# Kernel tuning notes

Measured on AMD Instinct MI355X. Metric: run time of the kernel, lower is better.

The kernel has to match this reference:

```python
import jax, jax.numpy as jnp
import numpy as np

NUM_ANCHORS = 3
NUM_CLASSES = 3
NUM_BB_ATTR = 9  # x, y, z, h, w, l, im, re, conf
EXP_CLAMP = 1000.0

_ANCHORS = np.array([[11.4, 8.6, 38.7, 0.0, 1.0],
                     [25.4, 11.2, 52.0, 0.0, 1.0],
                     [41.9, 16.2, 75.2, 0.0, 1.0]], dtype=np.float32)


def setup_inputs() -> dict:
    key = jax.random.key(0)
    B, G = 32, 152
    C = NUM_ANCHORS * (NUM_BB_ATTR + NUM_CLASSES)  # 36
    x = jax.random.normal(key, (B, C, G, G), dtype=jnp.float32)
    anchors = jnp.asarray(_ANCHORS)
    return {"x": x, "anchors": anchors, "img_size": 608}


def reference(x, anchors, img_size):
    B, _, G, _ = x.shape
    nA, nC, nbb = NUM_ANCHORS, NUM_CLASSES, NUM_BB_ATTR
    stride = jnp.asarray(img_size, x.dtype) / G

    # [B, nA, 9+nC, G, G] -> [B, nA, G, G, 9+nC]
    pred = x.reshape(B, nA, nbb + nC, G, G).transpose(0, 1, 3, 4, 2)

    pred_x = jax.nn.sigmoid(pred[..., 0])
    pred_y = jax.nn.sigmoid(pred[..., 1])
    pred_z = jax.nn.sigmoid(pred[..., 2])
    pred_h = pred[..., 3]
    pred_w = pred[..., 4]
    pred_l = pred[..., 5]
    pred_im = pred[..., 6]
    pred_re = pred[..., 7]
    pred_conf = jax.nn.sigmoid(pred[..., 8])
    pred_cls = jax.nn.sigmoid(pred[..., 9:])

    # grid offsets: grid_x varies along last (x) axis, grid_y along row axis
    g = jnp.arange(G, dtype=x.dtype)
    grid_x = g[None, None, None, :]   # [1,1,1,G] broadcasts over rows
    grid_y = g[None, None, :, None]   # [1,1,G,1] broadcasts over cols

    scaled = jnp.concatenate([anchors[:, :3] / stride, anchors[:, 3:]], axis=1)
    anchor_h = scaled[:, 0].reshape(1, nA, 1, 1)
    anchor_w = scaled[:, 1].reshape(1, nA, 1, 1)
    anchor_l = scaled[:, 2].reshape(1, nA, 1, 1)

    bx = pred_x + grid_x
    by = pred_y + grid_y
    bz = pred_z
    bh = jnp.minimum(jnp.exp(pred_h), EXP_CLAMP) * anchor_h
    bw = jnp.minimum(jnp.exp(pred_w), EXP_CLAMP) * anchor_w
    bl = jnp.minimum(jnp.exp(pred_l), EXP_CLAMP) * anchor_l

    N = nA * G * G
    flat = lambda t: t.reshape(B, N, 1)
    output = jnp.concatenate([
        flat(bx) * stride, flat(by) * stride,   # xy in image units
        flat(bz),
        flat(bh) * stride, flat(bw) * stride, flat(bl) * stride,
        flat(pred_im), flat(pred_re),
        flat(pred_conf),
        pred_cls.reshape(B, N, nC),
    ], axis=-1)  # [B, nA*G*G, 9+nC]
    return output
```

## Files before the change

kernel.cpp:

```cpp
#include <hip/hip_runtime.h>
#include <math.h>

#define GDIM 152
#define NA 3
#define GG (GDIM * GDIM)
#define EXP_CLAMP 1000.0f
#define NTHREADS 64
#define TILE 256
#define GSTRIDE (TILE + 1)

typedef float floatx4 __attribute__((ext_vector_type(4)));

__device__ __forceinline__ float sigmoidf(float v) {
    return 1.0f / (1.0f + __expf(-v));
}

__device__ __forceinline__ int swz(int e) { return e ^ ((e >> 3) & 7); }

__global__ __launch_bounds__(NTHREADS) void yolo_decode_w64(
    const float* __restrict__ x,
    const float* __restrict__ anchors,
    const int* __restrict__ img_size_p,
    float* __restrict__ out)
{
    __shared__ floatx4 sh[3 * GSTRIDE];

    const int t = threadIdx.x;
    const int tilebase = blockIdx.x * TILE;

    const float stride = (float)(*img_size_p) / (float)GDIM;
    const float inv_s = 1.0f / stride;

    const int cbase = tilebase + 4 * t;
    const unsigned t2 = (unsigned)cbase / (unsigned)GG;
    const int pos = cbase - (int)t2 * GG;
    const int gy  = pos / GDIM;
    const int gx0 = pos - gy * GDIM;
    const int a   = (int)(t2 % 3u);
    const float gyf = (float)gy;

    const floatx4* ip = (const floatx4*)x + (size_t)(t2 * 12u) * (GG / 4) + (pos >> 2);
    const int PS = GG / 4;

    floatx4 r0  = ip[0 * PS];
    floatx4 r1  = ip[1 * PS];
    floatx4 r2  = ip[2 * PS];
    floatx4 r3  = ip[3 * PS];
    floatx4 r4  = ip[4 * PS];
    floatx4 r5  = ip[5 * PS];
    floatx4 r6  = ip[6 * PS];
    floatx4 r7  = ip[7 * PS];
    floatx4 r8  = ip[8 * PS];
    floatx4 r9  = ip[9 * PS];
    floatx4 r10 = ip[10 * PS];
    floatx4 r11 = ip[11 * PS];

    const float ah = anchors[a * 5 + 0] * inv_s * stride;
    const float aw = anchors[a * 5 + 1] * inv_s * stride;
    const float al = anchors[a * 5 + 2] * inv_s * stride;

#define PROC(J, C)                                                       \
    do {                                                                 \
        floatx4 o0, o1, o2;                                              \
        o0.x = (sigmoidf(r0.C) + (float)(gx0 + J)) * stride;             \
        o0.y = (sigmoidf(r1.C) + gyf) * stride;                          \
        o0.z = sigmoidf(r2.C);                                           \
        o0.w = fminf(__expf(r3.C), EXP_CLAMP) * ah;                      \
        o1.x = fminf(__expf(r4.C), EXP_CLAMP) * aw;                      \
        o1.y = fminf(__expf(r5.C), EXP_CLAMP) * al;                      \
        o1.z = r6.C;                                                     \
        o1.w = r7.C;                                                     \
        o2.x = sigmoidf(r8.C);                                           \
        o2.y = sigmoidf(r9.C);                                           \
        o2.z = sigmoidf(r10.C);                                          \
        o2.w = sigmoidf(r11.C);                                          \
        int e = swz(4 * t + (J));                                        \
        sh[0 * GSTRIDE + e] = o0;                                        \
        sh[1 * GSTRIDE + e] = o1;                                        \
        sh[2 * GSTRIDE + e] = o2;                                        \
    } while (0)

    PROC(0, x);
    PROC(1, y);
    PROC(2, z);
    PROC(3, w);
#undef PROC

    __syncthreads();

    floatx4* op = (floatx4*)out + (size_t)tilebase * 3;
#pragma unroll
    for (int k = 0; k < 12; ++k) {
        int F = t + NTHREADS * k;
        unsigned cell = (unsigned)F / 3u;
        int g = F - (int)cell * 3;
        floatx4 v = sh[g * GSTRIDE + swz((int)cell)];
        __builtin_nontemporal_store(v, op + F);
    }
}

extern "C" void kernel_launch(void* const* d_in, const int* in_sizes, int n_in,
                              void* d_out, int out_size, void* d_ws, size_t ws_size,
                              hipStream_t stream) {
    const float* x        = (const float*)d_in[0];
    const float* anchors  = (const float*)d_in[1];
    const int*   img_size = (const int*)d_in[2];
    float*       out      = (float*)d_out;

    const int B = 32;
    const int total = B * NA * GG;
    const int grid = total / TILE;

    yolo_decode_w64<<<grid, NTHREADS, 0, stream>>>(x, anchors, img_size, out);
}
```

Measured before the change: 188.5 us.

## Process three tiles per block with register double-buffered prefetch

Each 64-thread block now handles three 256-cell tiles instead of one, loading the next tile's 12 input vectors into registers while the current tile is transposed through shared memory and stored. This is meant to hide global load latency within a block and cut per-block setup cost, such as the anchor loads and index math. The price is higher register pressure from two 12-vector buffers, a third of the blocks in the grid, and extra barriers per block.

```diff
diff --git a/kernel.cpp b/kernel.cpp
--- a/kernel.cpp
+++ b/kernel.cpp
@@ -8,6 +8,9 @@
 #define NTHREADS 64
 #define TILE 256
 #define GSTRIDE (TILE + 1)
+#define TILES_TOTAL 8664
+#define NTPB 3
+#define NBLK (TILES_TOTAL / NTPB)
 
 typedef float floatx4 __attribute__((ext_vector_type(4)));
 
@@ -17,7 +20,82 @@
 
 __device__ __forceinline__ int swz(int e) { return e ^ ((e >> 3) & 7); }
 
-__global__ __launch_bounds__(NTHREADS) void yolo_decode_w64(
+__device__ __forceinline__ const floatx4* make_ip(int tile, int t,
+                                                  const float* __restrict__ x) {
+    const int cbase = tile * TILE + 4 * t;
+    const unsigned t2 = (unsigned)cbase / (unsigned)GG;
+    const int pos = cbase - (int)t2 * GG;
+    return (const floatx4*)x + (size_t)(t2 * 12u) * (GG / 4) + (pos >> 2);
+}
+
+struct TileCtx {
+    floatx4* op;
+    float gx0f, gyf, ah, aw, al;
+};
+
+__device__ __forceinline__ TileCtx make_ctx(int tile, int t, float* __restrict__ out,
+        const float* atab ) {
+    TileCtx c;
+    const int tilebase = tile * TILE;
+    const int cbase = tilebase + 4 * t;
+    const unsigned t2 = (unsigned)cbase / (unsigned)GG;
+    const int pos = cbase - (int)t2 * GG;
+    const int gy = pos / GDIM;
+    const int gx0 = pos - gy * GDIM;
+    const int a = (int)(t2 % 3u);
+    c.gx0f = (float)gx0;
+    c.gyf  = (float)gy;
+    c.op   = (floatx4*)out + (size_t)tilebase * 3;
+    c.ah = (a == 0) ? atab[0] : (a == 1) ? atab[3] : atab[6];
+    c.aw = (a == 0) ? atab[1] : (a == 1) ? atab[4] : atab[7];
+    c.al = (a == 0) ? atab[2] : (a == 1) ? atab[5] : atab[8];
+    return c;
+}
+
+__device__ __forceinline__ void load12(const floatx4* __restrict__ ip, floatx4 r[12]) {
+    const int PS = GG / 4;
+#pragma unroll
+    for (int k = 0; k < 12; ++k) r[k] = ip[k * PS];
+}
+
+__device__ __forceinline__ void phase1(const TileCtx& c, const floatx4 r[12],
+                                       floatx4* sh, int t, float stride) {
+    __syncthreads();
+#pragma unroll
+    for (int J = 0; J < 4; ++J) {
+        floatx4 o0, o1, o2;
+        o0.x = (sigmoidf(r[0][J]) + c.gx0f + (float)J) * stride;
+        o0.y = (sigmoidf(r[1][J]) + c.gyf) * stride;
+        o0.z = sigmoidf(r[2][J]);
+        o0.w = fminf(__expf(r[3][J]), EXP_CLAMP) * c.ah;
+        o1.x = fminf(__expf(r[4][J]), EXP_CLAMP) * c.aw;
+        o1.y = fminf(__expf(r[5][J]), EXP_CLAMP) * c.al;
+        o1.z = r[6][J];
+        o1.w = r[7][J];
+        o2.x = sigmoidf(r[8][J]);
+        o2.y = sigmoidf(r[9][J]);
+        o2.z = sigmoidf(r[10][J]);
+        o2.w = sigmoidf(r[11][J]);
+        const int e = swz(4 * t + J);
+        sh[0 * GSTRIDE + e] = o0;
+        sh[1 * GSTRIDE + e] = o1;
+        sh[2 * GSTRIDE + e] = o2;
+    }
+}
+
+__device__ __forceinline__ void phase2(const TileCtx& c, const floatx4* sh, int t) {
+    __syncthreads();
+#pragma unroll
+    for (int k = 0; k < 12; ++k) {
+        const int F = t + NTHREADS * k;
+        const unsigned cell = (unsigned)F / 3u;
+        const int g = F - (int)cell * 3;
+        floatx4 v = sh[g * GSTRIDE + swz((int)cell)];
+        __builtin_nontemporal_store(v, c.op + F);
+    }
+}
+
+__global__ __launch_bounds__(NTHREADS) void yolo_decode_pipe(
     const float* __restrict__ x,
     const float* __restrict__ anchors,
     const int* __restrict__ img_size_p,
@@ -26,76 +104,44 @@
     __shared__ floatx4 sh[3 * GSTRIDE];
 
     const int t = threadIdx.x;
-    const int tilebase = blockIdx.x * TILE;
-
     const float stride = (float)(*img_size_p) / (float)GDIM;
     const float inv_s = 1.0f / stride;
 
-    const int cbase = tilebase + 4 * t;
-    const unsigned t2 = (unsigned)cbase / (unsigned)GG;
-    const int pos = cbase - (int)t2 * GG;
-    const int gy  = pos / GDIM;
-    const int gx0 = pos - gy * GDIM;
-    const int a   = (int)(t2 % 3u);
-    const float gyf = (float)gy;
+    float atab[9];
+#pragma unroll
+    for (int a = 0; a < 3; ++a) {
+#pragma unroll
+        for (int j = 0; j < 3; ++j)
+            atab[a * 3 + j] = anchors[a * 5 + j] * inv_s * stride;
+    }
 
-    const floatx4* ip = (const floatx4*)x + (size_t)(t2 * 12u) * (GG / 4) + (pos >> 2);
-    const int PS = GG / 4;
+    const int tA = blockIdx.x;
+    const int tB = tA + NBLK;
+    const int tC = tA + 2 * NBLK;
 
-    floatx4 r0  = ip[0 * PS];
-    floatx4 r1  = ip[1 * PS];
-    floatx4 r2  = ip[2 * PS];
-    floatx4 r3  = ip[3 * PS];
-    floatx4 r4  = ip[4 * PS];
-    floatx4 r5  = ip[5 * PS];
-    floatx4 r6  = ip[6 * PS];
-    floatx4 r7  = ip[7 * PS];
-    floatx4 r8  = ip[8 * PS];
-    floatx4 r9  = ip[9 * PS];
-    floatx4 r10 = ip[10 * PS];
-    floatx4 r11 = ip[11 * PS];
+    const floatx4* ipA = make_ip(tA, t, x);
+    const floatx4* ipB = make_ip(tB, t, x);
+    const floatx4* ipC = make_ip(tC, t, x);
 
-    const float ah = anchors[a * 5 + 0] * inv_s * stride;
-    const float aw = anchors[a * 5 + 1] * inv_s * stride;
-    const float al = anchors[a * 5 + 2] * inv_s * stride;
+    floatx4 ra[12], rb[12];
+    load12(ipA, ra);
+    load12(ipB, rb);
 
-#define PROC(J, C)                                                       \
-    do {                                                                 \
-        floatx4 o0, o1, o2;                                              \
-        o0.x = (sigmoidf(r0.C) + (float)(gx0 + J)) * stride;             \
-        o0.y = (sigmoidf(r1.C) + gyf) * stride;                          \
-        o0.z = sigmoidf(r2.C);                                           \
-        o0.w = fminf(__expf(r3.C), EXP_CLAMP) * ah;                      \
-        o1.x = fminf(__expf(r4.C), EXP_CLAMP) * aw;                      \
-        o1.y = fminf(__expf(r5.C), EXP_CLAMP) * al;                      \
-        o1.z = r6.C;                                                     \
-        o1.w = r7.C;                                                     \
-        o2.x = sigmoidf(r8.C);                                           \
-        o2.y = sigmoidf(r9.C);                                           \
-        o2.z = sigmoidf(r10.C);                                          \
-        o2.w = sigmoidf(r11.C);                                          \
-        int e = swz(4 * t + (J));                                        \
-        sh[0 * GSTRIDE + e] = o0;                                        \
-        sh[1 * GSTRIDE + e] = o1;                                        \
-        sh[2 * GSTRIDE + e] = o2;                                        \
-    } while (0)
-
-    PROC(0, x);
-    PROC(1, y);
-    PROC(2, z);
-    PROC(3, w);
-#undef PROC
-
-    __syncthreads();
-
-    floatx4* op = (floatx4*)out + (size_t)tilebase * 3;
-#pragma unroll
-    for (int k = 0; k < 12; ++k) {
-        int F = t + NTHREADS * k;
-        unsigned cell = (unsigned)F / 3u;
-        int g = F - (int)cell * 3;
-        floatx4 v = sh[g * GSTRIDE + swz((int)cell)];
-        __builtin_nontemporal_store(v, op + F);
+    {
+        TileCtx c = make_ctx(tA, t, out, atab);
+        phase1(c, ra, sh, t, stride);
+        load12(ipC, ra);
+        phase2(c, sh, t);
+    }
+    {
+        TileCtx c = make_ctx(tB, t, out, atab);
+        phase1(c, rb, sh, t, stride);
+        phase2(c, sh, t);
+    }
+    {
+        TileCtx c = make_ctx(tC, t, out, atab);
+        phase1(c, ra, sh, t, stride);
+        phase2(c, sh, t);
     }
 }
 
@@ -107,9 +153,5 @@
     const int*   img_size = (const int*)d_in[2];
     float*       out      = (float*)d_out;
 
-    const int B = 32;
-    const int total = B * NA * GG;
-    const int grid = total / TILE;
-
-    yolo_decode_w64<<<grid, NTHREADS, 0, stream>>>(x, anchors, img_size, out);
+    yolo_decode_pipe<<<NBLK, NTHREADS, 0, stream>>>(x, anchors, img_size, out);
 }
```

Result: slower. 193.7 us (+2.8%).

## Drop LDS transpose and store outputs directly with 8 cells per thread

Applied to the files above, without the earlier changes.

Removes the shared-memory staging and barrier. Each thread now handles 8 consecutive cells, loading two float4 per channel plane, and writes its 3×float4 output records straight to global memory with nontemporal stores. Block size grows to 256 threads with a launch-bounds occupancy hint. The direct stores are strided per lane (48-byte records, 384 bytes apart between lanes), so write coalescing may be worse than the old LDS-transposed contiguous stores. Register pressure also rises with 24 float4 held live.

```diff
diff --git a/kernel.cpp b/kernel.cpp
--- a/kernel.cpp
+++ b/kernel.cpp
@@ -5,9 +5,10 @@
 #define NA 3
 #define GG (GDIM * GDIM)
 #define EXP_CLAMP 1000.0f
-#define NTHREADS 64
-#define TILE 256
-#define GSTRIDE (TILE + 1)
+#define NTHREADS 256
+#define CPT 8
+#define CPB (NTHREADS * CPT)
+#define NBLK (32 * NA * GG / CPB)
 
 typedef float floatx4 __attribute__((ext_vector_type(4)));
 
@@ -15,87 +16,63 @@
     return 1.0f / (1.0f + __expf(-v));
 }
 
-__device__ __forceinline__ int swz(int e) { return e ^ ((e >> 3) & 7); }
-
-__global__ __launch_bounds__(NTHREADS) void yolo_decode_w64(
+__global__ __launch_bounds__(NTHREADS, 4) void yolo_decode_direct(
     const float* __restrict__ x,
     const float* __restrict__ anchors,
     const int* __restrict__ img_size_p,
     float* __restrict__ out)
 {
-    __shared__ floatx4 sh[3 * GSTRIDE];
-
-    const int t = threadIdx.x;
-    const int tilebase = blockIdx.x * TILE;
-
-    const float stride = (float)(*img_size_p) / (float)GDIM;
-    const float inv_s = 1.0f / stride;
-
-    const int cbase = tilebase + 4 * t;
+    const int T = blockIdx.x * NTHREADS + threadIdx.x;
+    const int cbase = T * CPT;
     const unsigned t2 = (unsigned)cbase / (unsigned)GG;
     const int pos = cbase - (int)t2 * GG;
     const int gy  = pos / GDIM;
     const int gx0 = pos - gy * GDIM;
     const int a   = (int)(t2 % 3u);
-    const float gyf = (float)gy;
+
+    const float stride = (float)(*img_size_p) / (float)GDIM;
+    const float inv_s  = 1.0f / stride;
 
     const floatx4* ip = (const floatx4*)x + (size_t)(t2 * 12u) * (GG / 4) + (pos >> 2);
     const int PS = GG / 4;
 
-    floatx4 r0  = ip[0 * PS];
-    floatx4 r1  = ip[1 * PS];
-    floatx4 r2  = ip[2 * PS];
-    floatx4 r3  = ip[3 * PS];
-    floatx4 r4  = ip[4 * PS];
-    floatx4 r5  = ip[5 * PS];
-    floatx4 r6  = ip[6 * PS];
-    floatx4 r7  = ip[7 * PS];
-    floatx4 r8  = ip[8 * PS];
-    floatx4 r9  = ip[9 * PS];
-    floatx4 r10 = ip[10 * PS];
-    floatx4 r11 = ip[11 * PS];
+    floatx4 r[24];
+#pragma unroll
+    for (int p = 0; p < 12; ++p) {
+        r[2 * p]     = ip[p * PS];
+        r[2 * p + 1] = ip[p * PS + 1];
+    }
 
     const float ah = anchors[a * 5 + 0] * inv_s * stride;
     const float aw = anchors[a * 5 + 1] * inv_s * stride;
     const float al = anchors[a * 5 + 2] * inv_s * stride;
+    const float gyf = (float)gy;
 
-#define PROC(J, C)                                                       \
-    do {                                                                 \
-        floatx4 o0, o1, o2;                                              \
-        o0.x = (sigmoidf(r0.C) + (float)(gx0 + J)) * stride;             \
-        o0.y = (sigmoidf(r1.C) + gyf) * stride;                          \
-        o0.z = sigmoidf(r2.C);                                           \
-        o0.w = fminf(__expf(r3.C), EXP_CLAMP) * ah;                      \
-        o1.x = fminf(__expf(r4.C), EXP_CLAMP) * aw;                      \
-        o1.y = fminf(__expf(r5.C), EXP_CLAMP) * al;                      \
-        o1.z = r6.C;                                                     \
-        o1.w = r7.C;                                                     \
-        o2.x = sigmoidf(r8.C);                                           \
-        o2.y = sigmoidf(r9.C);                                           \
-        o2.z = sigmoidf(r10.C);                                          \
-        o2.w = sigmoidf(r11.C);                                          \
-        int e = swz(4 * t + (J));                                        \
-        sh[0 * GSTRIDE + e] = o0;                                        \
-        sh[1 * GSTRIDE + e] = o1;                                        \
-        sh[2 * GSTRIDE + e] = o2;                                        \
-    } while (0)
+    floatx4* op = (floatx4*)out + (size_t)cbase * 3;
 
-    PROC(0, x);
-    PROC(1, y);
-    PROC(2, z);
-    PROC(3, w);
-#undef PROC
+#pragma unroll
+    for (int h = 0; h < 2; ++h) {
+#pragma unroll
+        for (int J = 0; J < 4; ++J) {
+            floatx4 o0, o1, o2;
+            o0.x = (sigmoidf(r[0 * 2 + h][J]) + (float)(gx0 + 4 * h + J)) * stride;
+            o0.y = (sigmoidf(r[1 * 2 + h][J]) + gyf) * stride;
+            o0.z = sigmoidf(r[2 * 2 + h][J]);
+            o0.w = fminf(__expf(r[3 * 2 + h][J]), EXP_CLAMP) * ah;
+            o1.x = fminf(__expf(r[4 * 2 + h][J]), EXP_CLAMP) * aw;
+            o1.y = fminf(__expf(r[5 * 2 + h][J]), EXP_CLAMP) * al;
+            o1.z = r[6 * 2 + h][J];
+            o1.w = r[7 * 2 + h][J];
+            o2.x = sigmoidf(r[8 * 2 + h][J]);
+            o2.y = sigmoidf(r[9 * 2 + h][J]);
+            o2.z = sigmoidf(r[10 * 2 + h][J]);
+            o2.w = sigmoidf(r[11 * 2 + h][J]);
 
-    __syncthreads();
-
-    floatx4* op = (floatx4*)out + (size_t)tilebase * 3;
-#pragma unroll
-    for (int k = 0; k < 12; ++k) {
-        int F = t + NTHREADS * k;
-        unsigned cell = (unsigned)F / 3u;
-        int g = F - (int)cell * 3;
-        floatx4 v = sh[g * GSTRIDE + swz((int)cell)];
-        __builtin_nontemporal_store(v, op + F);
+            const int cell = 4 * h + J;
+            __builtin_nontemporal_store(o0, op + cell * 3 + 0);
+            __builtin_nontemporal_store(o1, op + cell * 3 + 1);
+            __builtin_nontemporal_store(o2, op + cell * 3 + 2);
+        }
     }
 }
 
@@ -107,9 +84,5 @@
     const int*   img_size = (const int*)d_in[2];
     float*       out      = (float*)d_out;
 
-    const int B = 32;
-    const int total = B * NA * GG;
-    const int grid = total / TILE;
-
-    yolo_decode_w64<<<grid, NTHREADS, 0, stream>>>(x, anchors, img_size, out);
+    yolo_decode_direct<<<NBLK, NTHREADS, 0, stream>>>(x, anchors, img_size, out);
 }
```

Result: slower. 444.2 us (+135.7%).

## Process four tiles per block with double-buffered register prefetch of inputs

Applied to the files above, without the earlier changes.

The grid shrinks to a quarter of its former size. Each block now handles four tiles spaced 24 (batch, anchor) planes apart, so the grid position and anchor index stay valid for every tile. Two register buffers of 12 channel vectors are loaded ahead, so global loads for the next tiles are in flight while the current tile is decoded, transposed through LDS and stored. The aim is to hide memory latency and raise achieved bandwidth. In exchange it uses more registers, adds extra barriers, and replaces the nontemporal output stores with ordinary stores, which may change cache behaviour.

```diff
diff --git a/kernel.cpp b/kernel.cpp
--- a/kernel.cpp
+++ b/kernel.cpp
@@ -8,6 +8,11 @@
 #define NTHREADS 64
 #define TILE 256
 #define GSTRIDE (TILE + 1)
+#define TILES_TOTAL 8664
+#define NTPB 4
+#define NBLK (TILES_TOTAL / NTPB)
+#define ISTEP ((size_t)24 * 12 * (GG / 4))
+#define OSTEP ((size_t)NBLK * TILE * 3)
 
 typedef float floatx4 __attribute__((ext_vector_type(4)));
 
@@ -17,7 +22,7 @@
 
 __device__ __forceinline__ int swz(int e) { return e ^ ((e >> 3) & 7); }
 
-__global__ __launch_bounds__(NTHREADS) void yolo_decode_w64(
+__global__ __launch_bounds__(NTHREADS) void yolo_decode_pers(
     const float* __restrict__ x,
     const float* __restrict__ anchors,
     const int* __restrict__ img_size_p,
@@ -39,64 +44,69 @@
     const int a   = (int)(t2 % 3u);
     const float gyf = (float)gy;
 
-    const floatx4* ip = (const floatx4*)x + (size_t)(t2 * 12u) * (GG / 4) + (pos >> 2);
     const int PS = GG / 4;
-
-    floatx4 r0  = ip[0 * PS];
-    floatx4 r1  = ip[1 * PS];
-    floatx4 r2  = ip[2 * PS];
-    floatx4 r3  = ip[3 * PS];
-    floatx4 r4  = ip[4 * PS];
-    floatx4 r5  = ip[5 * PS];
-    floatx4 r6  = ip[6 * PS];
-    floatx4 r7  = ip[7 * PS];
-    floatx4 r8  = ip[8 * PS];
-    floatx4 r9  = ip[9 * PS];
-    floatx4 r10 = ip[10 * PS];
-    floatx4 r11 = ip[11 * PS];
+    const floatx4* ip = (const floatx4*)x + (size_t)(t2 * 12u) * PS + (pos >> 2);
+    floatx4* op = (floatx4*)out + (size_t)tilebase * 3;
 
     const float ah = anchors[a * 5 + 0] * inv_s * stride;
     const float aw = anchors[a * 5 + 1] * inv_s * stride;
     const float al = anchors[a * 5 + 2] * inv_s * stride;
 
-#define PROC(J, C)                                                       \
+#define PROCJ(R, J)                                                      \
     do {                                                                 \
         floatx4 o0, o1, o2;                                              \
-        o0.x = (sigmoidf(r0.C) + (float)(gx0 + J)) * stride;             \
-        o0.y = (sigmoidf(r1.C) + gyf) * stride;                          \
-        o0.z = sigmoidf(r2.C);                                           \
-        o0.w = fminf(__expf(r3.C), EXP_CLAMP) * ah;                      \
-        o1.x = fminf(__expf(r4.C), EXP_CLAMP) * aw;                      \
-        o1.y = fminf(__expf(r5.C), EXP_CLAMP) * al;                      \
-        o1.z = r6.C;                                                     \
-        o1.w = r7.C;                                                     \
-        o2.x = sigmoidf(r8.C);                                           \
-        o2.y = sigmoidf(r9.C);                                           \
-        o2.z = sigmoidf(r10.C);                                          \
-        o2.w = sigmoidf(r11.C);                                          \
+        o0.x = (sigmoidf(R[0][J]) + (float)(gx0 + (J))) * stride;        \
+        o0.y = (sigmoidf(R[1][J]) + gyf) * stride;                       \
+        o0.z = sigmoidf(R[2][J]);                                        \
+        o0.w = fminf(__expf(R[3][J]), EXP_CLAMP) * ah;                   \
+        o1.x = fminf(__expf(R[4][J]), EXP_CLAMP) * aw;                   \
+        o1.y = fminf(__expf(R[5][J]), EXP_CLAMP) * al;                   \
+        o1.z = R[6][J];                                                  \
+        o1.w = R[7][J];                                                  \
+        o2.x = sigmoidf(R[8][J]);                                        \
+        o2.y = sigmoidf(R[9][J]);                                        \
+        o2.z = sigmoidf(R[10][J]);                                       \
+        o2.w = sigmoidf(R[11][J]);                                       \
         int e = swz(4 * t + (J));                                        \
         sh[0 * GSTRIDE + e] = o0;                                        \
         sh[1 * GSTRIDE + e] = o1;                                        \
         sh[2 * GSTRIDE + e] = o2;                                        \
     } while (0)
 
-    PROC(0, x);
-    PROC(1, y);
-    PROC(2, z);
-    PROC(3, w);
-#undef PROC
+#define COMPUTE_STORE(R)                                                 \
+    do {                                                                 \
+        __syncthreads();                                                 \
+        PROCJ(R, 0); PROCJ(R, 1); PROCJ(R, 2); PROCJ(R, 3);              \
+        __syncthreads();                                                 \
+        _Pragma("unroll")                                                \
+        for (int k2 = 0; k2 < 12; ++k2) {                                \
+            int F = t + NTHREADS * k2;                                   \
+            unsigned cell = (unsigned)F / 3u;                            \
+            int g = F - (int)cell * 3;                                   \
+            op[F] = sh[g * GSTRIDE + swz((int)cell)];                    \
+        }                                                                \
+        op += OSTEP;                                                     \
+    } while (0)
 
-    __syncthreads();
+    floatx4 ra[12], rb[12];
+#pragma unroll
+    for (int k = 0; k < 12; ++k) ra[k] = ip[k * PS];
+    ip += ISTEP;
+#pragma unroll
+    for (int k = 0; k < 12; ++k) rb[k] = ip[k * PS];
+    ip += ISTEP;
 
-    floatx4* op = (floatx4*)out + (size_t)tilebase * 3;
+    COMPUTE_STORE(ra);
 #pragma unroll
-    for (int k = 0; k < 12; ++k) {
-        int F = t + NTHREADS * k;
-        unsigned cell = (unsigned)F / 3u;
-        int g = F - (int)cell * 3;
-        floatx4 v = sh[g * GSTRIDE + swz((int)cell)];
-        __builtin_nontemporal_store(v, op + F);
-    }
+    for (int k = 0; k < 12; ++k) ra[k] = ip[k * PS];
+    ip += ISTEP;
+
+    COMPUTE_STORE(rb);
+#pragma unroll
+    for (int k = 0; k < 12; ++k) rb[k] = ip[k * PS];
+
+    COMPUTE_STORE(ra);
+    COMPUTE_STORE(rb);
 }
 
 extern "C" void kernel_launch(void* const* d_in, const int* in_sizes, int n_in,
@@ -107,9 +117,5 @@
     const int*   img_size = (const int*)d_in[2];
     float*       out      = (float*)d_out;
 
-    const int B = 32;
-    const int total = B * NA * GG;
-    const int grid = total / TILE;
-
-    yolo_decode_w64<<<grid, NTHREADS, 0, stream>>>(x, anchors, img_size, out);
+    yolo_decode_pers<<<NBLK, NTHREADS, 0, stream>>>(x, anchors, img_size, out);
 }
```

After: 192.8 us. 2.3% more time.
